# Kernel optimization log

Measured on AMD Instinct MI355X. Metric: run time of the kernel, lower is better.

## Reference

```python
import jax, jax.numpy as jnp
import numpy as np
from jax import lax

WIDTH = 512
NUM_STEPS = 100
BATCH = 128


def setup_inputs() -> dict:
    key = jax.random.key(0)
    strokes = jax.random.uniform(key, (BATCH, 10), dtype=jnp.float32)
    return {"strokes": strokes}


def _forward(strokes):
    B = strokes.shape[0]
    width = WIDTH
    sigma = 0.5

    # 3x3 gaussian blur kernel (matches torch.meshgrid default 'ij' indexing)
    ax = jnp.arange(-1, 2, dtype=jnp.float32)
    gx, gy = jnp.meshgrid(ax, ax, indexing="ij")
    k = jnp.exp(-(gx ** 2 + gy ** 2) / (2.0 * sigma ** 2))
    blur = (k / jnp.sum(k))[None, None, :, :]  # [1,1,3,3]

    xs = jnp.arange(width, dtype=jnp.float32)
    grid_x, grid_y = jnp.meshgrid(xs, xs, indexing="ij")  # [W,W]

    t = jnp.linspace(0.0, 1.0, NUM_STEPS, dtype=jnp.float32)
    mt = 1.0 - t
    qbc_start = mt ** 2
    qbc_middle = 2.0 * mt * t
    qbc_stop = t ** 2

    scale = lambda v: v * (width - 1) + 0.5
    P0 = strokes[:, 0:2]
    P1 = strokes[:, 2:4]
    P2 = strokes[:, 4:6]
    P1 = P0 + (P2 - P0) * P1
    P0, P1, P2 = scale(P0), scale(P1), scale(P2)

    radii = 1.0 + strokes[:, 6:8] * (width // 4)
    radius0, radius2 = radii[:, 0], radii[:, 1]
    color0, color2 = strokes[:, 8], strokes[:, 9]

    # quadratic Bezier trajectory: [B, T, 2]
    P = (jnp.einsum("bd,t->btd", P0, qbc_start)
         + jnp.einsum("bd,t->btd", P1, qbc_middle)
         + jnp.einsum("bd,t->btd", P2, qbc_stop))
    X, Y = P[..., 0], P[..., 1]                      # [B,T]
    radius = radius0[:, None] * mt + radius2[:, None] * t  # [B,T]
    color = color0[:, None] * mt + color2[:, None] * t     # [B,T]

    def step(canvas, xs_t):
        Xt, Yt, rt, ct = xs_t  # each [B]
        dist2 = ((grid_x[None] - Xt[:, None, None]) ** 2
                 + (grid_y[None] - Yt[:, None, None]) ** 2)
        mask = dist2 < rt[:, None, None] ** 2
        canvas = jnp.where(mask, ct[:, None, None], canvas)
        return canvas, None

    canvas0 = jnp.zeros((B, width, width), dtype=jnp.float32)
    canvas, _ = lax.scan(step, canvas0, (X.T, Y.T, radius.T, color.T))

    # 3x3 blur with padding=1 (SAME)
    canvas = lax.conv_general_dilated(
        canvas[:, None, :, :], blur, window_strides=(1, 1),
        padding=((1, 1), (1, 1)),
        dimension_numbers=("NCHW", "OIHW", "NCHW"))[:, 0]
    return 1.0 - canvas


def reference(strokes):
    return _forward(strokes)
```

## Files before the change

### kernel.cpp

```cpp
#include <hip/hip_runtime.h>

#define W      512
#define NSTEP  100
#define OUTH   14
#define RROWS  16
#define NTILE  37
#define CSTRB  520
#define SEGW   32

__global__ __launch_bounds__(256) void qbc_kernel(
    const float* __restrict__ strokes, float* __restrict__ out, int B)
{
    #pragma clang fp contract(off)

    const int b   = blockIdx.y;
    const int R0  = blockIdx.x * OUTH;
    const int tid = threadIdx.x;

    __shared__ float4 steps[NSTEP];
    __shared__ float4 clist[NSTEP];
    __shared__ int    flags[NSTEP];
    __shared__ int    nlist;
    __shared__ float  colors[NSTEP + 1];
    __shared__ int    ivl[NSTEP * RROWS];
    __shared__ __align__(16) unsigned char cbytes[RROWS * CSTRB];

    {
        uint4 z = make_uint4(0u, 0u, 0u, 0u);
        uint4* p = (uint4*)cbytes;
        for (int i = tid; i < (RROWS * CSTRB) / 16; i += 256) p[i] = z;
    }

    if (tid < NSTEP) {
        const float* s = strokes + b * 10;
        float P0x = s[0], P0y = s[1];
        float m1x = s[2], m1y = s[3];
        float P2x = s[4], P2y = s[5];
        float P1x = P0x + (P2x - P0x) * m1x;
        float P1y = P0y + (P2y - P0y) * m1y;
        float X0 = P0x * 511.0f + 0.5f;
        float X1 = P1x * 511.0f + 0.5f;
        float X2 = P2x * 511.0f + 0.5f;
        float Y0 = P0y * 511.0f + 0.5f;
        float Y1 = P1y * 511.0f + 0.5f;
        float Y2 = P2y * 511.0f + 0.5f;
        float r0 = 1.0f + s[6] * 128.0f;
        float r2 = 1.0f + s[7] * 128.0f;
        float c0 = s[8], c2 = s[9];
        float tf = (float)tid * (1.0f / 99.0f);
        float mt = 1.0f - tf;
        float s0 = mt * mt;
        float s1 = (2.0f * mt) * tf;
        float s2 = tf * tf;
        float ex0 = X0 * s0, ex1 = X1 * s1, ex2 = X2 * s2;
        float X   = (ex0 + ex1) + ex2;
        float ey0 = Y0 * s0, ey1 = Y1 * s1, ey2 = Y2 * s2;
        float Y   = (ey0 + ey1) + ey2;
        float ra  = r0 * mt, rb = r2 * tf;
        float rt  = ra + rb;
        float r2t = rt * rt;
        float ca  = c0 * mt, cb = c2 * tf;
        float ct  = ca + cb;
        steps[tid] = make_float4(X, Y, r2t, ct);

        float lo_i = (float)(R0 - 1), hi_i = (float)(R0 + OUTH);
        float ci = fminf(fmaxf(X, lo_i), hi_i);
        float di = X - ci;
        flags[tid] = ((di * di) < (r2t + 4.0f)) ? 1 : 0;
    }
    __syncthreads();

    if (tid < 64) {
        bool f0 = flags[tid] != 0;
        unsigned long long m0 = __ballot(f0);
        int p0 = __popcll(m0 & ((1ull << tid) - 1ull));
        if (f0) { float4 v = steps[tid]; clist[p0] = v; colors[p0 + 1] = v.w; }
        int cnt = __popcll(m0);
        int t1 = 64 + tid;
        bool f1 = (t1 < NSTEP) && (flags[t1] != 0);
        unsigned long long m1 = __ballot(f1);
        int p1 = __popcll(m1 & ((1ull << tid) - 1ull));
        if (f1) { float4 v = steps[t1]; clist[cnt + p1] = v; colors[cnt + p1 + 1] = v.w; }
        if (tid == 0) { nlist = cnt + __popcll(m1); colors[0] = 0.0f; }
    }
    __syncthreads();
    const int n = nlist;

    for (int job = tid; job < n * RROWS; job += 256) {
        int k   = job >> 4;
        int row = job & (RROWS - 1);
        float4 st = clist[k];
        float X = st.x, Y = st.y, r2 = st.z;
        int gi = R0 - 1 + row;
        float fi = (float)gi;
        float dx  = fi - X;
        float dxq = dx * dx;
        int packed = 1;
        float T = r2 - dxq;
        if (T >= -0.375f) {
            auto ehit = [&](int j) -> bool {
                float dy  = (float)j - Y;
                float dyq = dy * dy;
                float d2  = dxq + dyq;
                return d2 < r2;
            };
            float s_in = (T > 0.375f) ? sqrtf(T - 0.375f) : 0.0f;
            int gl = (int)ceilf (Y - s_in);
            int gh = (int)floorf(Y + s_in);
            int jlo, jhi; bool ok;
            if (gh - gl >= 4) {
                jlo = ehit(gl - 1) ? gl - 1 : (ehit(gl) ? gl : gl + 1);
                jhi = ehit(gh + 1) ? gh + 1 : (ehit(gh) ? gh : gh - 1);
                ok = true;
            } else {
                jlo = 1; jhi = 0; ok = false;
                for (int j = gl - 1; j <= gh + 1; ++j)
                    if (ehit(j)) { if (!ok) { jlo = j; ok = true; } jhi = j; }
            }
            if (ok) packed = (jhi << 16) | (jlo & 0xffff);
        }
        ivl[k * RROWS + row] = packed;
    }

    const int seg = tid & 15;
    const int row = tid >> 4;
    const int gi  = R0 - 1 + row;
    const int c0i = seg * SEGW;
    unsigned char* crow = &cbytes[row * CSTRB + 1];
    __syncthreads();

    unsigned int undone = (gi >= 0 && gi < W) ? ~0u : 0u;
    int packed = (n > 0) ? ivl[(n - 1) * RROWS + row] : 1;
    for (int k = n - 1; k >= 0; --k) {
        if (__all(undone == 0u)) break;
        int nxt = (k > 0) ? ivl[(k - 1) * RROWS + row] : 1;
        if (undone) {
            int jlo = (int)(short)(packed & 0xffff);
            int jhi = packed >> 16;
            int lo = jlo > c0i ? jlo : c0i;
            int hi = jhi < c0i + SEGW - 1 ? jhi : c0i + SEGW - 1;
            if (lo <= hi) {
                unsigned int m = (~0u >> (31 - (hi - c0i))) & (~0u << (lo - c0i));
                unsigned int paint = m & undone;
                undone &= ~m;
                unsigned char id = (unsigned char)(k + 1);
                while (paint) {
                    int j = __builtin_ctz(paint);
                    paint &= paint - 1;
                    crow[c0i + j] = id;
                }
            }
        }
        packed = nxt;
    }
    __syncthreads();

    const float A    = 0.13533528323661270f;
    const double Ad  = 0.13533528323661270;
    const float INVS = (float)(1.0 / ((1.0 + 2.0 * Ad) * (1.0 + 2.0 * Ad)));

    const int j0 = tid << 1;
    auto hrow = [&](int rr) -> float2 {
        const unsigned char* rb = &cbytes[rr * CSTRB];
        unsigned int w0 = *(const unsigned short*)(rb + j0);
        unsigned int w1 = *(const unsigned short*)(rb + j0 + 2);
        float x0 = colors[w0 & 0xffu];
        float x1 = colors[w0 >> 8];
        float x2 = colors[w1 & 0xffu];
        float x3 = colors[w1 >> 8];
        return make_float2(x1 + A * (x0 + x2), x2 + A * (x1 + x3));
    };

    float2 hp = hrow(0);
    float2 hm = hrow(1);
    for (int orow = 0; orow < OUTH; ++orow) {
        float2 hn = hrow(orow + 2);
        int grow = R0 + orow;
        if (grow < W) {
            float2 o;
            o.x = 1.0f - (hm.x + A * (hp.x + hn.x)) * INVS;
            o.y = 1.0f - (hm.y + A * (hp.y + hn.y)) * INVS;
            *reinterpret_cast<float2*>(&out[((size_t)b * W + grow) * W + j0]) = o;
        }
        hp = hm; hm = hn;
    }
}

extern "C" void kernel_launch(void* const* d_in, const int* in_sizes, int n_in,
                              void* d_out, int out_size, void* d_ws, size_t ws_size,
                              hipStream_t stream) {
    const float* strokes = (const float*)d_in[0];
    float* out = (float*)d_out;
    int B = in_sizes[0] / 10;
    dim3 grid(NTILE, B);
    qbc_kernel<<<grid, dim3(256), 0, stream>>>(strokes, out, B);
}
```

Measured before the change: 168.0 us.

## Store fp16 colors in LDS canvas and transpose interval table for vector loads

The shared canvas now holds fp16 color values directly instead of byte step IDs, so the blur pass no longer does an indirect lookup into a color table. The interval table is transposed to row-major, and the paint loop reads four steps at once with an int4 load, unrolled by four. In exchange, the canvas uses twice as much LDS and colors are rounded to fp16, which adds a small precision error in the output.

```diff
diff --git a/kernel.cpp b/kernel.cpp
--- a/kernel.cpp
+++ b/kernel.cpp
@@ -5,7 +5,7 @@
 #define OUTH   14
 #define RROWS  16
 #define NTILE  37
-#define CSTRB  520
+#define HSTR   520
 #define SEGW   32
 
 __global__ __launch_bounds__(256) void qbc_kernel(
@@ -19,16 +19,16 @@
 
     __shared__ float4 steps[NSTEP];
     __shared__ float4 clist[NSTEP];
+    __shared__ float  colors[NSTEP];
     __shared__ int    flags[NSTEP];
     __shared__ int    nlist;
-    __shared__ float  colors[NSTEP + 1];
-    __shared__ int    ivl[NSTEP * RROWS];
-    __shared__ __align__(16) unsigned char cbytes[RROWS * CSTRB];
+    __shared__ __align__(16) int ivl[RROWS * NSTEP];
+    __shared__ __align__(16) _Float16 hcanvas[RROWS * HSTR];
 
     {
         uint4 z = make_uint4(0u, 0u, 0u, 0u);
-        uint4* p = (uint4*)cbytes;
-        for (int i = tid; i < (RROWS * CSTRB) / 16; i += 256) p[i] = z;
+        uint4* p = (uint4*)hcanvas;
+        for (int i = tid; i < (RROWS * HSTR * 2) / 16; i += 256) p[i] = z;
     }
 
     if (tid < NSTEP) {
@@ -74,25 +74,25 @@
         bool f0 = flags[tid] != 0;
         unsigned long long m0 = __ballot(f0);
         int p0 = __popcll(m0 & ((1ull << tid) - 1ull));
-        if (f0) { float4 v = steps[tid]; clist[p0] = v; colors[p0 + 1] = v.w; }
+        if (f0) clist[p0] = steps[tid];
         int cnt = __popcll(m0);
         int t1 = 64 + tid;
         bool f1 = (t1 < NSTEP) && (flags[t1] != 0);
         unsigned long long m1 = __ballot(f1);
         int p1 = __popcll(m1 & ((1ull << tid) - 1ull));
-        if (f1) { float4 v = steps[t1]; clist[cnt + p1] = v; colors[cnt + p1 + 1] = v.w; }
-        if (tid == 0) { nlist = cnt + __popcll(m1); colors[0] = 0.0f; }
+        if (f1) clist[cnt + p1] = steps[t1];
+        if (tid == 0) nlist = cnt + __popcll(m1);
     }
     __syncthreads();
     const int n = nlist;
 
     for (int job = tid; job < n * RROWS; job += 256) {
-        int k   = job >> 4;
-        int row = job & (RROWS - 1);
+        int k  = job >> 4;
+        int rw = job & (RROWS - 1);
         float4 st = clist[k];
         float X = st.x, Y = st.y, r2 = st.z;
-        int gi = R0 - 1 + row;
-        float fi = (float)gi;
+        int gi_ = R0 - 1 + rw;
+        float fi = (float)gi_;
         float dx  = fi - X;
         float dxq = dx * dx;
         int packed = 1;
@@ -119,39 +119,47 @@
             }
             if (ok) packed = (jhi << 16) | (jlo & 0xffff);
         }
-        ivl[k * RROWS + row] = packed;
+        ivl[rw * NSTEP + k] = packed;
+        if (rw == 0) colors[k] = st.w;
     }
 
     const int seg = tid & 15;
     const int row = tid >> 4;
     const int gi  = R0 - 1 + row;
     const int c0i = seg * SEGW;
-    unsigned char* crow = &cbytes[row * CSTRB + 1];
+    _Float16* crow = &hcanvas[row * HSTR + 1];
+    const int* ivlrow = &ivl[row * NSTEP];
     __syncthreads();
 
     unsigned int undone = (gi >= 0 && gi < W) ? ~0u : 0u;
-    int packed = (n > 0) ? ivl[(n - 1) * RROWS + row] : 1;
-    for (int k = n - 1; k >= 0; --k) {
-        if (__all(undone == 0u)) break;
-        int nxt = (k > 0) ? ivl[(k - 1) * RROWS + row] : 1;
-        if (undone) {
-            int jlo = (int)(short)(packed & 0xffff);
-            int jhi = packed >> 16;
-            int lo = jlo > c0i ? jlo : c0i;
-            int hi = jhi < c0i + SEGW - 1 ? jhi : c0i + SEGW - 1;
-            if (lo <= hi) {
-                unsigned int m = (~0u >> (31 - (hi - c0i))) & (~0u << (lo - c0i));
-                unsigned int paint = m & undone;
-                undone &= ~m;
-                unsigned char id = (unsigned char)(k + 1);
-                while (paint) {
-                    int j = __builtin_ctz(paint);
-                    paint &= paint - 1;
-                    crow[c0i + j] = id;
-                }
+
+    auto dostep = [&](int packed, int k) {
+        if (k >= n || !undone) return;
+        int jlo = (int)(short)(packed & 0xffff);
+        int jhi = packed >> 16;
+        int lo = jlo > c0i ? jlo : c0i;
+        int hi = jhi < c0i + SEGW - 1 ? jhi : c0i + SEGW - 1;
+        if (lo > hi) return;
+        unsigned int m = (~0u >> (31 - (hi - c0i))) & (~0u << (lo - c0i));
+        unsigned int paint = m & undone;
+        undone &= ~m;
+        if (paint) {
+            _Float16 hc = (_Float16)colors[k];
+            while (paint) {
+                int j = __builtin_ctz(paint);
+                paint &= paint - 1;
+                crow[c0i + j] = hc;
             }
         }
-        packed = nxt;
+    };
+
+    for (int kc = ((n + 3) & ~3) - 4; kc >= 0; kc -= 4) {
+        if (__all(undone == 0u)) break;
+        int4 q = *(const int4*)&ivlrow[kc];
+        dostep(q.w, kc + 3);
+        dostep(q.z, kc + 2);
+        dostep(q.y, kc + 1);
+        dostep(q.x, kc + 0);
     }
     __syncthreads();
 
@@ -161,13 +169,12 @@
 
     const int j0 = tid << 1;
     auto hrow = [&](int rr) -> float2 {
-        const unsigned char* rb = &cbytes[rr * CSTRB];
-        unsigned int w0 = *(const unsigned short*)(rb + j0);
-        unsigned int w1 = *(const unsigned short*)(rb + j0 + 2);
-        float x0 = colors[w0 & 0xffu];
-        float x1 = colors[w0 >> 8];
-        float x2 = colors[w1 & 0xffu];
-        float x3 = colors[w1 >> 8];
+        const unsigned int* p = (const unsigned int*)&hcanvas[rr * HSTR + j0];
+        unsigned int u0 = p[0], u1 = p[1];
+        float x0 = (float)__builtin_bit_cast(_Float16, (unsigned short)(u0 & 0xffffu));
+        float x1 = (float)__builtin_bit_cast(_Float16, (unsigned short)(u0 >> 16));
+        float x2 = (float)__builtin_bit_cast(_Float16, (unsigned short)(u1 & 0xffffu));
+        float x3 = (float)__builtin_bit_cast(_Float16, (unsigned short)(u1 >> 16));
         return make_float2(x1 + A * (x0 + x2), x2 + A * (x1 + x3));
     };
 
```

New measurement: 171.0 us. Within noise of the previous version (+1.8%).

## Cull occluded stroke intervals per row and paint survivors with wide stores

Applied to the files above, without the earlier changes.

The interval table is transposed to row-major. One thread per row then walks the steps from last to first and drops intervals already fully covered by the running union of later intervals, compacting the survivors with their step ids. The paint phase replaces the back-to-front per-pixel undone-mask loop with a front-to-back painter's pass that fills each segment using aligned 1/2/4/8-byte stores. This is meant to cut per-pixel ctz stores and per-step mask work, but it adds a serial 16-thread culling pass and may overdraw pixels that the old mask skipped.

```diff
diff --git a/kernel.cpp b/kernel.cpp
--- a/kernel.cpp
+++ b/kernel.cpp
@@ -1,4 +1,5 @@
 #include <hip/hip_runtime.h>
+#include <stdint.h>
 
 #define W      512
 #define NSTEP  100
@@ -19,10 +20,11 @@
 
     __shared__ float4 steps[NSTEP];
     __shared__ float4 clist[NSTEP];
+    __shared__ float  colors[NSTEP + 1];
     __shared__ int    flags[NSTEP];
     __shared__ int    nlist;
-    __shared__ float  colors[NSTEP + 1];
-    __shared__ int    ivl[NSTEP * RROWS];
+    __shared__ int    scnt[RROWS];
+    __shared__ __align__(16) int ivl[RROWS * NSTEP];
     __shared__ __align__(16) unsigned char cbytes[RROWS * CSTRB];
 
     {
@@ -87,12 +89,12 @@
     const int n = nlist;
 
     for (int job = tid; job < n * RROWS; job += 256) {
-        int k   = job >> 4;
-        int row = job & (RROWS - 1);
+        int k  = job >> 4;
+        int rw = job & (RROWS - 1);
         float4 st = clist[k];
         float X = st.x, Y = st.y, r2 = st.z;
-        int gi = R0 - 1 + row;
-        float fi = (float)gi;
+        int gi_ = R0 - 1 + rw;
+        float fi = (float)gi_;
         float dx  = fi - X;
         float dxq = dx * dx;
         int packed = 1;
@@ -119,39 +121,66 @@
             }
             if (ok) packed = (jhi << 16) | (jlo & 0xffff);
         }
-        ivl[k * RROWS + row] = packed;
+        ivl[rw * NSTEP + k] = packed;
+    }
+    __syncthreads();
+
+    if (tid < RROWS) {
+        int r = tid;
+        int gi_ = R0 - 1 + r;
+        int cnt = 0;
+        if (gi_ >= 0 && gi_ < W) {
+            int wp  = NSTEP - 1;
+            int ulo = 1 << 29, uhi = -(1 << 29);
+            int* rowivl = &ivl[r * NSTEP];
+            for (int k = n - 1; k >= 0; --k) {
+                int e = rowivl[k];
+                int jlo = (int)(short)(e & 0xffff);
+                int jhi = e >> 16;
+                jlo = jlo > 0 ? jlo : 0;
+                jhi = jhi < (W - 1) ? jhi : (W - 1);
+                if (jlo > jhi) continue;
+                if (jlo >= ulo && jhi <= uhi) continue;
+                rowivl[wp--] = (k << 20) | ((jhi + 256) << 10) | (jlo + 256);
+                ++cnt;
+                if (jlo > uhi + 1 || jhi < ulo - 1) {
+                    if (jhi - jlo > uhi - ulo) { ulo = jlo; uhi = jhi; }
+                } else { ulo = ulo < jlo ? ulo : jlo; uhi = uhi > jhi ? uhi : jhi; }
+            }
+        }
+        scnt[r] = cnt;
     }
 
     const int seg = tid & 15;
     const int row = tid >> 4;
-    const int gi  = R0 - 1 + row;
     const int c0i = seg * SEGW;
-    unsigned char* crow = &cbytes[row * CSTRB + 1];
-    __syncthreads();
-
-    unsigned int undone = (gi >= 0 && gi < W) ? ~0u : 0u;
-    int packed = (n > 0) ? ivl[(n - 1) * RROWS + row] : 1;
-    for (int k = n - 1; k >= 0; --k) {
-        if (__all(undone == 0u)) break;
-        int nxt = (k > 0) ? ivl[(k - 1) * RROWS + row] : 1;
-        if (undone) {
-            int jlo = (int)(short)(packed & 0xffff);
-            int jhi = packed >> 16;
-            int lo = jlo > c0i ? jlo : c0i;
-            int hi = jhi < c0i + SEGW - 1 ? jhi : c0i + SEGW - 1;
-            if (lo <= hi) {
-                unsigned int m = (~0u >> (31 - (hi - c0i))) & (~0u << (lo - c0i));
-                unsigned int paint = m & undone;
-                undone &= ~m;
-                unsigned char id = (unsigned char)(k + 1);
-                while (paint) {
-                    int j = __builtin_ctz(paint);
-                    paint &= paint - 1;
-                    crow[c0i + j] = id;
-                }
-            }
-        }
-        packed = nxt;
+    unsigned char* rowb = &cbytes[row * CSTRB + 1];
+    __syncthreads();
+
+    {
+        const int cnt  = scnt[row];
+        const int base = NSTEP - cnt;
+        const int* rowivl = &ivl[row * NSTEP];
+        for (int i = 0; i < cnt; ++i) {
+            int e   = rowivl[base + i];
+            int jlo = (e & 0x3ff) - 256;
+            int jhi = ((e >> 10) & 0x3ff) - 256;
+            int lo  = jlo > c0i ? jlo : c0i;
+            int hi  = jhi < c0i + SEGW - 1 ? jhi : c0i + SEGW - 1;
+            if (lo > hi) continue;
+            unsigned int id = (unsigned int)(e >> 20) + 1u;
+            unsigned int cc = id * 0x01010101u;
+            unsigned long long cc2 = ((unsigned long long)cc << 32) | cc;
+            unsigned char* p = rowb + lo;
+            int len = hi - lo + 1;
+            if (((uintptr_t)p & 1) && len)        { *p = (unsigned char)id; p += 1; len -= 1; }
+            if (((uintptr_t)p & 2) && len >= 2)   { *(unsigned short*)p = (unsigned short)cc; p += 2; len -= 2; }
+            if (((uintptr_t)p & 4) && len >= 4)   { *(unsigned int*)p = cc; p += 4; len -= 4; }
+            while (len >= 8) { *(unsigned long long*)p = cc2; p += 8; len -= 8; }
+            if (len >= 4)    { *(unsigned int*)p = cc; p += 4; len -= 4; }
+            if (len >= 2)    { *(unsigned short*)p = (unsigned short)cc; p += 2; len -= 2; }
+            if (len)         { *p = (unsigned char)id; }
+        }
     }
     __syncthreads();
 
```

After: 201.8 us. 20.1% more time.
